# Kernel tuning notes

Hardware: AMD Instinct MI355X
Metric: run time of the kernel (lower is better)

The kernel has to match this reference:

```python
import jax, jax.numpy as jnp
import numpy as np

K = 5          # kernel_size
BETA = 15.0    # soft-max temperature
SOFT_MAX = True
OP_TYPE = 'dilation2d'  # or 'erosion2d'
OUT_CHANNELS = 1


def _fixed_padding(x, k):
    pad_total = k - 1
    pb = pad_total // 2
    pe = pad_total - pb
    # torch 'replicate' == jnp 'edge'
    return jnp.pad(x, ((0, 0), (0, 0), (pb, pe), (pb, pe)), mode='edge')


def _one_iter(x):
    B, C, H, W = x.shape
    xp = _fixed_padding(x, K)
    # im2col: (B, C, K*K, H, W) -> (B, C*K*K, H, W); channel-major then row-major
    # kernel offsets, matching nn.Unfold layout along dim 1.
    patches = jnp.stack(
        [xp[:, :, i:i + H, j:j + W] for i in range(K) for j in range(K)], axis=2
    ).reshape(B, C * K * K, H, W)
    if OP_TYPE == 'erosion2d':
        patches = -patches
    if SOFT_MAX:
        out = jax.nn.logsumexp(patches * BETA, axis=1) / BETA  # (B, H, W)
    else:
        out = jnp.max(patches, axis=1)
    if OP_TYPE == 'erosion2d':
        out = -out
    return out.reshape(-1, OUT_CHANNELS, H, W)


def setup_inputs() -> dict:
    key = jax.random.key(0)
    x = jax.random.normal(key, (4, 1, 1024, 1024), dtype=jnp.float32)
    return {"x": x, "iterations": 1}


def reference(x, iterations):
    for _ in range(iterations):
        x = _one_iter(x)
    return x
```

## Files before the change

kernel.cpp:

```cpp
#include <hip/hip_runtime.h>


constexpr int TW = 64;
constexpr int TH = 16;
constexpr int IW = TW + 4;
constexpr int IH = TH + 4;
constexpr int HH = 1024, WW = 1024;

__global__ __launch_bounds__(256)
void morph_lse_kernel(const float* __restrict__ x, float* __restrict__ out) {
    __shared__ float E[IH][IW];
    __shared__ float HS[IH][TW];

    const float SCALE = 21.6404256133f;
    const float SHIFT = 40.0f;
    const float INV   = 0.0462098120833f;

    const int bx = blockIdx.x, by = blockIdx.y, b = blockIdx.z;
    const int gx0 = bx * TW - 2;
    const int gy0 = by * TH - 2;
    const float* xb = x + (size_t)b * HH * WW;
    const int t = threadIdx.x;

    for (int idx = t; idx < IH * IW; idx += 256) {
        const int r = idx / IW;
        const int c = idx - r * IW;
        int gy = gy0 + r; gy = max(0, min(HH - 1, gy));
        int gx = gx0 + c; gx = max(0, min(WW - 1, gx));
        const float v = xb[gy * WW + gx];
        E[r][c] = exp2f(fmaf(v, SCALE, -SHIFT));
    }
    __syncthreads();

    const int c  = t & 63;
    const int r0 = t >> 6;
    for (int r = r0; r < IH; r += 4) {
        HS[r][c] = E[r][c] + E[r][c + 1] + E[r][c + 2] + E[r][c + 3] + E[r][c + 4];
    }
    __syncthreads();

    float* ob = out + (size_t)b * HH * WW;
    #pragma unroll
    for (int i = 0; i < TH / 4; ++i) {
        const int hr = r0 + 4 * i;
        const float s = HS[hr][c] + HS[hr + 1][c] + HS[hr + 2][c]
                      + HS[hr + 3][c] + HS[hr + 4][c];
        ob[(size_t)(by * TH + hr) * WW + bx * TW + c] =
            (log2f(s) + SHIFT) * INV;
    }
}

extern "C" void kernel_launch(void* const* d_in, const int* in_sizes, int n_in,
                              void* d_out, int out_size, void* d_ws, size_t ws_size,
                              hipStream_t stream) {
    const float* x = (const float*)d_in[0];
    float* out = (float*)d_out;
    dim3 grid(WW / TW, HH / TH, 4);
    morph_lse_kernel<<<grid, dim3(256), 0, stream>>>(x, out);
}
```

Measured before the change: 15.77 us.

## Vectorize halo loads and stores, fuse separable box sum into registers

Interior blocks now load the tile with aligned float4 global reads and float2 shared stores, and edge blocks keep the clamped scalar path. The separate horizontal-sum shared buffer and its barrier are removed: each thread computes four adjacent outputs directly from 5 rows of float4 shared reads with shared partial sums, then writes them with one float4 store. This cuts load and store instruction count and one synchronization, at the cost of a branchy load path and more shared reads per output.

```diff
diff --git a/kernel.cpp b/kernel.cpp
--- a/kernel.cpp
+++ b/kernel.cpp
@@ -3,51 +3,73 @@
 
 constexpr int TW = 64;
 constexpr int TH = 16;
-constexpr int IW = TW + 4;
+constexpr int IW = 72;
 constexpr int IH = TH + 4;
 constexpr int HH = 1024, WW = 1024;
 
 __global__ __launch_bounds__(256)
 void morph_lse_kernel(const float* __restrict__ x, float* __restrict__ out) {
     __shared__ float E[IH][IW];
-    __shared__ float HS[IH][TW];
 
     const float SCALE = 21.6404256133f;
     const float SHIFT = 40.0f;
     const float INV   = 0.0462098120833f;
 
     const int bx = blockIdx.x, by = blockIdx.y, b = blockIdx.z;
-    const int gx0 = bx * TW - 2;
+    const int t = threadIdx.x;
     const int gy0 = by * TH - 2;
     const float* xb = x + (size_t)b * HH * WW;
-    const int t = threadIdx.x;
 
-    for (int idx = t; idx < IH * IW; idx += 256) {
-        const int r = idx / IW;
-        const int c = idx - r * IW;
-        int gy = gy0 + r; gy = max(0, min(HH - 1, gy));
-        int gx = gx0 + c; gx = max(0, min(WW - 1, gx));
-        const float v = xb[gy * WW + gx];
-        E[r][c] = exp2f(fmaf(v, SCALE, -SHIFT));
+    if (bx >= 1 && bx <= WW / TW - 2) {
+        for (int idx = t; idx < IH * 18; idx += 256) {
+            const int r = idx / 18;
+            const int m = idx - r * 18;
+            int gy = gy0 + r; gy = max(0, min(HH - 1, gy));
+            const float4 v = *reinterpret_cast<const float4*>(
+                xb + (size_t)gy * WW + bx * TW - 4 + 4 * m);
+            const float e0 = exp2f(fmaf(v.x, SCALE, -SHIFT));
+            const float e1 = exp2f(fmaf(v.y, SCALE, -SHIFT));
+            const float e2 = exp2f(fmaf(v.z, SCALE, -SHIFT));
+            const float e3 = exp2f(fmaf(v.w, SCALE, -SHIFT));
+            if (m >= 1)
+                *reinterpret_cast<float2*>(&E[r][4 * m - 2]) = make_float2(e0, e1);
+            *reinterpret_cast<float2*>(&E[r][4 * m]) = make_float2(e2, e3);
+        }
+    } else {
+        for (int idx = t; idx < IH * 68; idx += 256) {
+            const int r = idx / 68;
+            const int c = idx - r * 68;
+            int gy = gy0 + r; gy = max(0, min(HH - 1, gy));
+            int gx = bx * TW - 2 + c; gx = max(0, min(WW - 1, gx));
+            E[r][c] = exp2f(fmaf(xb[(size_t)gy * WW + gx], SCALE, -SHIFT));
+        }
     }
     __syncthreads();
 
-    const int c  = t & 63;
-    const int r0 = t >> 6;
-    for (int r = r0; r < IH; r += 4) {
-        HS[r][c] = E[r][c] + E[r][c + 1] + E[r][c + 2] + E[r][c + 3] + E[r][c + 4];
+    const int r  = t >> 4;
+    const int c0 = (t & 15) * 4;
+    float a0 = 0.f, a1 = 0.f, a2 = 0.f, a3 = 0.f;
+    #pragma unroll
+    for (int rr = 0; rr < 5; ++rr) {
+        const float4 u = *reinterpret_cast<const float4*>(&E[r + rr][c0]);
+        const float4 w = *reinterpret_cast<const float4*>(&E[r + rr][c0 + 4]);
+        const float p1 = u.y + u.z;
+        const float p3 = u.w + w.x;
+        const float p5 = w.y + w.z;
+        const float M  = p1 + p3;
+        a0 += u.x + M;
+        a1 += M + w.y;
+        a2 += u.z + p3 + p5;
+        a3 += p3 + p5 + w.w;
     }
-    __syncthreads();
-
+    float4 o;
+    o.x = (log2f(a0) + SHIFT) * INV;
+    o.y = (log2f(a1) + SHIFT) * INV;
+    o.z = (log2f(a2) + SHIFT) * INV;
+    o.w = (log2f(a3) + SHIFT) * INV;
     float* ob = out + (size_t)b * HH * WW;
-    #pragma unroll
-    for (int i = 0; i < TH / 4; ++i) {
-        const int hr = r0 + 4 * i;
-        const float s = HS[hr][c] + HS[hr + 1][c] + HS[hr + 2][c]
-                      + HS[hr + 3][c] + HS[hr + 4][c];
-        ob[(size_t)(by * TH + hr) * WW + bx * TW + c] =
-            (log2f(s) + SHIFT) * INV;
-    }
+    *reinterpret_cast<float4*>(
+        ob + (size_t)(by * TH + r) * WW + bx * TW + c0) = o;
 }
 
 extern "C" void kernel_launch(void* const* d_in, const int* in_sizes, int n_in,
```

Result: slower. 17.64 us (+11.9%).

## Enlarge tile, compute horizontal sums in registers with vectorized loads and stores

Applied to the files above, without the earlier changes.

Grows the tile to 64x64 with 512 threads, which shrinks the halo overhead per output. Each thread now does four float4 loads per row segment and computes the exponentials and the 5-wide horizontal sums in registers. This removes the exp staging array and one barrier. The vertical sum reads float4 from shared memory, uses hardware exp2 and log intrinsics with a folded offset, and writes float4 outputs. Edge tiles keep a clamped scalar path, and the tile count drops to 1024 blocks, so the GPU has fewer blocks to keep busy.

```diff
diff --git a/kernel.cpp b/kernel.cpp
--- a/kernel.cpp
+++ b/kernel.cpp
@@ -2,51 +2,83 @@
 
 
 constexpr int TW = 64;
-constexpr int TH = 16;
-constexpr int IW = TW + 4;
-constexpr int IH = TH + 4;
+constexpr int TH = 64;
+constexpr int HR = TH + 4;
+constexpr int HSTR = 72;
 constexpr int HH = 1024, WW = 1024;
 
-__global__ __launch_bounds__(256)
+__global__ __launch_bounds__(512)
 void morph_lse_kernel(const float* __restrict__ x, float* __restrict__ out) {
-    __shared__ float E[IH][IW];
-    __shared__ float HS[IH][TW];
+    __shared__ float HS[HR][HSTR];
 
     const float SCALE = 21.6404256133f;
     const float SHIFT = 40.0f;
     const float INV   = 0.0462098120833f;
+    const float OFS   = 1.84839248333f;
 
     const int bx = blockIdx.x, by = blockIdx.y, b = blockIdx.z;
-    const int gx0 = bx * TW - 2;
-    const int gy0 = by * TH - 2;
+    const int t = threadIdx.x;
+    const int R0 = by * TH, C0 = bx * TW;
     const float* xb = x + (size_t)b * HH * WW;
-    const int t = threadIdx.x;
+    const bool interior = (bx >= 1) && (bx <= WW / TW - 2);
 
-    for (int idx = t; idx < IH * IW; idx += 256) {
-        const int r = idx / IW;
-        const int c = idx - r * IW;
-        int gy = gy0 + r; gy = max(0, min(HH - 1, gy));
-        int gx = gx0 + c; gx = max(0, min(WW - 1, gx));
-        const float v = xb[gy * WW + gx];
-        E[r][c] = exp2f(fmaf(v, SCALE, -SHIFT));
+    for (int idx = t; idx < HR * 8; idx += 512) {
+        const int rr = idx >> 3;
+        const int g  = idx & 7;
+        int gy = R0 - 2 + rr;
+        gy = max(0, min(HH - 1, gy));
+        const float* row = xb + (size_t)gy * WW;
+        const int cb = C0 + g * 8 - 2;
+        float e[12];
+        if (interior) {
+            const float4 v0 = *reinterpret_cast<const float4*>(row + cb - 2);
+            const float4 v1 = *reinterpret_cast<const float4*>(row + cb + 2);
+            const float4 v2 = *reinterpret_cast<const float4*>(row + cb + 6);
+            const float4 v3 = *reinterpret_cast<const float4*>(row + cb + 10);
+            e[0] = v0.z;  e[1] = v0.w;
+            e[2] = v1.x;  e[3] = v1.y;  e[4] = v1.z;  e[5] = v1.w;
+            e[6] = v2.x;  e[7] = v2.y;  e[8] = v2.z;  e[9] = v2.w;
+            e[10] = v3.x; e[11] = v3.y;
+        } else {
+            #pragma unroll
+            for (int k = 0; k < 12; ++k) {
+                int gx = cb + k; gx = max(0, min(WW - 1, gx));
+                e[k] = row[gx];
+            }
+        }
+        #pragma unroll
+        for (int k = 0; k < 12; ++k)
+            e[k] = __builtin_amdgcn_exp2f(fmaf(e[k], SCALE, -SHIFT));
+        float p[11], q[8], h[8];
+        #pragma unroll
+        for (int k = 0; k < 11; ++k) p[k] = e[k] + e[k + 1];
+        #pragma unroll
+        for (int k = 0; k < 8; ++k)  q[k] = p[k] + e[k + 2];
+        #pragma unroll
+        for (int j = 0; j < 8; ++j)  h[j] = q[j] + p[j + 3];
+        *reinterpret_cast<float4*>(&HS[rr][g * 8])     = make_float4(h[0], h[1], h[2], h[3]);
+        *reinterpret_cast<float4*>(&HS[rr][g * 8 + 4]) = make_float4(h[4], h[5], h[6], h[7]);
     }
     __syncthreads();
 
-    const int c  = t & 63;
-    const int r0 = t >> 6;
-    for (int r = r0; r < IH; r += 4) {
-        HS[r][c] = E[r][c] + E[r][c + 1] + E[r][c + 2] + E[r][c + 3] + E[r][c + 4];
-    }
-    __syncthreads();
-
+    const int r0 = t >> 4;
+    const int c0 = (t & 15) * 4;
     float* ob = out + (size_t)b * HH * WW;
     #pragma unroll
-    for (int i = 0; i < TH / 4; ++i) {
-        const int hr = r0 + 4 * i;
-        const float s = HS[hr][c] + HS[hr + 1][c] + HS[hr + 2][c]
-                      + HS[hr + 3][c] + HS[hr + 4][c];
-        ob[(size_t)(by * TH + hr) * WW + bx * TW + c] =
-            (log2f(s) + SHIFT) * INV;
+    for (int u = 0; u < 2; ++u) {
+        const int r = r0 + u * 32;
+        float4 a = *reinterpret_cast<const float4*>(&HS[r][c0]);
+        #pragma unroll
+        for (int rr = 1; rr < 5; ++rr) {
+            const float4 v = *reinterpret_cast<const float4*>(&HS[r + rr][c0]);
+            a.x += v.x; a.y += v.y; a.z += v.z; a.w += v.w;
+        }
+        float4 o;
+        o.x = fmaf(__builtin_amdgcn_logf(a.x), INV, OFS);
+        o.y = fmaf(__builtin_amdgcn_logf(a.y), INV, OFS);
+        o.z = fmaf(__builtin_amdgcn_logf(a.z), INV, OFS);
+        o.w = fmaf(__builtin_amdgcn_logf(a.w), INV, OFS);
+        *reinterpret_cast<float4*>(ob + (size_t)(R0 + r) * WW + C0 + c0) = o;
     }
 }
 
@@ -56,5 +88,5 @@
     const float* x = (const float*)d_in[0];
     float* out = (float*)d_out;
     dim3 grid(WW / TW, HH / TH, 4);
-    morph_lse_kernel<<<grid, dim3(256), 0, stream>>>(x, out);
+    morph_lse_kernel<<<grid, dim3(512), 0, stream>>>(x, out);
 }
```

Measured after the change: 19.91 us. +26.2%, slower.
